# Kernel tuning notes

Measured on AMD Instinct MI355X. Metric: run time of the kernel, lower is better.

Reference implementation:

```python
import jax, jax.numpy as jnp
import numpy as np

EMBED_DIM = 1024
NUM_HEADS = 16
HEAD_DIM = EMBED_DIM // NUM_HEADS
KERNEL = 3
PAD = KERNEL // 2
B, L = 4, 1024


def conv1d(x, w, b):
    # x: [B, D, L], w: [D_out, D_in, K], b: [D_out]; 'same' padding like nn.Conv1d(padding=K//2)
    y = jax.lax.conv_general_dilated(
        x, w, window_strides=(1,), padding=[(PAD, PAD)],
        dimension_numbers=('NCH', 'OIH', 'NCH'))
    return y + b[None, :, None]


def setup_inputs() -> dict:
    key = jax.random.key(0)
    ks = jax.random.split(key, 12)
    fan = EMBED_DIM * KERNEL
    bound = 1.0 / np.sqrt(fan)
    def wconv(k):
        return jax.random.uniform(k, (EMBED_DIM, EMBED_DIM, KERNEL), jnp.float32, -bound, bound)
    def bconv(k):
        return jax.random.uniform(k, (EMBED_DIM,), jnp.float32, -bound, bound)
    return {
        'query': jax.random.normal(ks[0], (B, L, EMBED_DIM), jnp.float32),
        'key': jax.random.normal(ks[1], (B, L, EMBED_DIM), jnp.float32),
        'value': jax.random.normal(ks[2], (B, L, EMBED_DIM), jnp.float32),
        'key_padding_mask': jax.random.randint(ks[3], (B, L), 0, 2) > 0,
        'attn_mask': jnp.zeros((L, L), jnp.float32),
        'q_w': wconv(ks[4]), 'q_b': bconv(ks[5]),
        'k_w': wconv(ks[6]), 'k_b': bconv(ks[7]),
        'v_w': wconv(ks[8]), 'v_b': bconv(ks[9]),
        'o_w': wconv(ks[10]), 'o_b': bconv(ks[11]),
    }


def reference(query, key, value, key_padding_mask, attn_mask,
              q_w, q_b, k_w, k_b, v_w, v_b, o_w, o_b):
    scale = HEAD_DIM ** -0.5
    # projections: [B, D, L]
    q = conv1d(jnp.swapaxes(query, 1, 2), q_w, q_b)
    k = conv1d(jnp.swapaxes(key, 1, 2), k_w, k_b)
    v = conv1d(jnp.swapaxes(value, 1, 2), v_w, v_b)
    # [B, H, d, L]
    q = q.reshape(B, NUM_HEADS, HEAD_DIM, L)
    k = k.reshape(B, NUM_HEADS, HEAD_DIM, L)
    v = v.reshape(B, NUM_HEADS, HEAD_DIM, L)
    # scores: [B, H, L, L]
    scores = jnp.einsum('bhdi,bhdj->bhij', q, k) * scale
    scores = scores + attn_mask[None, None, :, :]
    scores = jnp.where(key_padding_mask[:, None, None, :], -jnp.inf, scores)
    attn = jax.nn.softmax(scores, axis=-1)  # dropout p=0 (eval) -> identity
    out = jnp.einsum('bhij,bhdj->bhdi', attn, v)  # [B, H, d, L]
    out = out.reshape(B, EMBED_DIM, L)
    out = conv1d(out, o_w, o_b)
    return jnp.swapaxes(out, 1, 2)  # [B, L, D]
```

## Files before the change

### kernel.cpp

```cpp
#include <hip/hip_runtime.h>
#include <math.h>

#define NB 4
#define NL 1024
#define ND 1024
#define NH 16
#define HD 64

typedef __attribute__((ext_vector_type(8))) short bf16x8;
typedef __attribute__((ext_vector_type(4))) float f32x4;

static __device__ __forceinline__ unsigned short f32_to_bf16(float f) {
  unsigned u = __float_as_uint(f);
  u += 0x7FFFu + ((u >> 16) & 1u);
  return (unsigned short)(u >> 16);
}
static __device__ __forceinline__ float bf16_to_f32(unsigned short s) {
  return __uint_as_float(((unsigned)s) << 16);
}

static __device__ __forceinline__ void split8(float4 a, float4 b, bf16x8* hi, bf16x8* lo) {
  unsigned u[8] = {__float_as_uint(a.x), __float_as_uint(a.y),
                   __float_as_uint(a.z), __float_as_uint(a.w),
                   __float_as_uint(b.x), __float_as_uint(b.y),
                   __float_as_uint(b.z), __float_as_uint(b.w)};
  union { unsigned p[4]; bf16x8 v; } H, L;
#pragma unroll
  for (int p = 0; p < 4; ++p) {
    unsigned u0 = u[2 * p], u1 = u[2 * p + 1];
    H.p[p] = __builtin_amdgcn_perm(u1, u0, 0x07060302u);
    unsigned l0 = __float_as_uint(__uint_as_float(u0) - __uint_as_float(u0 & 0xFFFF0000u));
    unsigned l1 = __float_as_uint(__uint_as_float(u1) - __uint_as_float(u1 & 0xFFFF0000u));
    L.p[p] = __builtin_amdgcn_perm(l1, l0, 0x07060302u);
  }
  *hi = H.v; *lo = L.v;
}

__global__ __launch_bounds__(256) void wcvt_kernel(
    const float* __restrict__ w0, const float* __restrict__ w1,
    const float* __restrict__ w2, const float* __restrict__ w3,
    unsigned short* __restrict__ wb, int* __restrict__ flag)
{
  if (blockIdx.x == 0 && blockIdx.y == 0 && threadIdx.x == 0) flag[0] = 0;
  const int t = blockIdx.y;
  const int o = blockIdx.x;
  const float* w = (t == 0) ? w0 : (t == 1) ? w1 : (t == 2) ? w2 : w3;
  unsigned short* hi = wb + (size_t)t * 6 * (1u << 20);
  unsigned short* lo = hi + 3 * (1u << 20);
  const int tid = threadIdx.x;
  float v[12];
  const float* src = w + (size_t)o * (ND * 3) + tid * 12;
#pragma unroll
  for (int j = 0; j < 3; ++j) {
    float4 f = *(const float4*)(src + j * 4);
    v[j * 4 + 0] = f.x; v[j * 4 + 1] = f.y; v[j * 4 + 2] = f.z; v[j * 4 + 3] = f.w;
  }
#pragma unroll
  for (int k = 0; k < 3; ++k) {
    unsigned short hh[4], ll[4];
#pragma unroll
    for (int ii = 0; ii < 4; ++ii) {
      float x = v[ii * 3 + k];
      unsigned short h = f32_to_bf16(x);
      float r = x - bf16_to_f32(h);
      hh[ii] = h; ll[ii] = f32_to_bf16(r);
    }
    size_t dst = (size_t)k * (ND * ND) + (size_t)o * ND + tid * 4;
    *(ushort4*)&hi[dst] = make_ushort4(hh[0], hh[1], hh[2], hh[3]);
    *(ushort4*)&lo[dst] = make_ushort4(ll[0], ll[1], ll[2], ll[3]);
  }
}

__global__ __launch_bounds__(256) void amask_scan(
    const float* __restrict__ a, int* __restrict__ flag)
{
  size_t i = ((size_t)blockIdx.x * 256 + threadIdx.x) * 4;
  float4 v = *(const float4*)&a[i];
  if (v.x != 0.f || v.y != 0.f || v.z != 0.f || v.w != 0.f) atomicOr(flag, 1);
}

__global__ __launch_bounds__(256, 3) void conv_mfma2(
    const float* X0, const float* X1, const float* X2,
    const unsigned short* __restrict__ wb,
    const float* b0, const float* b1, const float* b2,
    float* Y0, float* Y1, float* Y2, int mode)
{
  __shared__ float Af[128 * 32];
  __shared__ unsigned short Bh[128 * 32];
  __shared__ unsigned short Bl[128 * 32];

  const int tid = threadIdx.x, lane = tid & 63, wave = tid >> 6;
  const int lin = blockIdx.x + 8 * (blockIdx.y + 32 * blockIdx.z);
  const int g = lin & 7, t = lin >> 3;
  const int nb = (g & 3) * 2 + (t & 1);
  const int mb = (g >> 2) * 16 + ((t >> 1) & 15);
  const int z  = t >> 5;
  const int n0 = nb * 128, m0 = mb * 128;
  const int b = m0 >> 10, l0v = m0 & (NL - 1);

  const float* X = (mode == 0) ? (z == 0 ? X0 : (z == 1 ? X1 : X2)) : X0;
  const unsigned short* Wh = (mode == 0) ? wb + (size_t)z * 6 * (1u << 20) : wb;
  const unsigned short* Wl = Wh + 3 * (1u << 20);

  const int wm = (wave >> 1) * 64, wn = (wave & 1) * 64;
  const int mrow = lane & 15, quad = lane >> 4;
  const int r16 = lane >> 2, cs = lane & 3;
  const int src_chunk = (cs - (r16 >> 1)) & 3;
  const int bswz = ((quad + (mrow >> 1)) & 3) * 8;

  f32x4 acc[4][4] = {};

  const int kbeg = (mode == 0) ? 0 : z;
  const int kend = (mode == 0) ? 3 : z + 1;
  for (int koff = kbeg; koff < kend; ++koff) {
    const bool edge_lo = (l0v == 0 && koff == 0);
    const bool edge_hi = (l0v == NL - 128 && koff == 2);
    for (int i0 = 0; i0 < ND; i0 += 32) {
#pragma unroll
      for (int s = 0; s < 2; ++s) {
        const int seg = wave * 2 + s;
        const size_t goff = ((size_t)koff << 20) +
                            (size_t)(n0 + seg * 16 + r16) * ND + i0 + src_chunk * 8;
        __builtin_amdgcn_global_load_lds(
            (const __attribute__((address_space(1))) unsigned int*)(Wh + goff),
            (__attribute__((address_space(3))) unsigned int*)&Bh[seg * 512], 16, 0, 0);
        __builtin_amdgcn_global_load_lds(
            (const __attribute__((address_space(1))) unsigned int*)(Wl + goff),
            (__attribute__((address_space(3))) unsigned int*)&Bl[seg * 512], 16, 0, 0);
      }
#pragma unroll
      for (int j = 0; j < 4; ++j) {
        const int s = (wave * 4 + j) * 64 + lane;
        const int row = s >> 3, sir = s & 7;
        const int chunk = (sir - (row & 7)) & 7;
        int l = l0v + row + koff - 1;
        l = (l < 0) ? 0 : (l > NL - 1 ? NL - 1 : l);
        const float* gp = X + ((size_t)(b << 10) + l) * ND + i0 + chunk * 4;
        __builtin_amdgcn_global_load_lds(
            (const __attribute__((address_space(1))) unsigned int*)gp,
            (__attribute__((address_space(3))) unsigned int*)&Af[(wave * 4 + j) * 256],
            16, 0, 0);
      }
      __syncthreads();
      if (edge_lo || edge_hi) {
        const int er = edge_lo ? 0 : 127;
        if (tid < 8) *(float4*)&Af[er * 32 + tid * 4] = make_float4(0.f, 0.f, 0.f, 0.f);
        __syncthreads();
      }
      bf16x8 ah[4], al[4];
#pragma unroll
      for (int mi = 0; mi < 4; ++mi) {
        const int row = wm + mi * 16 + mrow, r7 = row & 7;
        float4 fa = *(const float4*)&Af[row * 32 + (((quad * 2) + r7) & 7) * 4];
        float4 fb = *(const float4*)&Af[row * 32 + (((quad * 2 + 1) + r7) & 7) * 4];
        split8(fa, fb, &ah[mi], &al[mi]);
      }
#pragma unroll
      for (int ni = 0; ni < 4; ++ni) {
        const int brow = wn + ni * 16 + mrow;
        bf16x8 bh = *(const bf16x8*)&Bh[brow * 32 + bswz];
        bf16x8 bl = *(const bf16x8*)&Bl[brow * 32 + bswz];
#pragma unroll
        for (int mi = 0; mi < 4; ++mi) {
          acc[mi][ni] = __builtin_amdgcn_mfma_f32_16x16x32_bf16(ah[mi], bh, acc[mi][ni], 0, 0, 0);
          acc[mi][ni] = __builtin_amdgcn_mfma_f32_16x16x32_bf16(ah[mi], bl, acc[mi][ni], 0, 0, 0);
          acc[mi][ni] = __builtin_amdgcn_mfma_f32_16x16x32_bf16(al[mi], bh, acc[mi][ni], 0, 0, 0);
        }
      }
      __syncthreads();
    }
  }

  if (mode == 0) {
    float* Y = (z == 0) ? Y0 : (z == 1 ? Y1 : Y2);
    const float* bias = (z == 0) ? b0 : (z == 1 ? b1 : b2);
#pragma unroll
    for (int ni = 0; ni < 4; ++ni) {
      const int n = n0 + wn + ni * 16 + mrow;
      const float bv = bias[n];
      const int h = n >> 6, dd = n & 63;
#pragma unroll
      for (int mi = 0; mi < 4; ++mi) {
        const int mbase = m0 + wm + mi * 16 + quad * 4;
        f32x4 v = acc[mi][ni];
#pragma unroll
        for (int r = 0; r < 4; ++r) {
          const int l = (mbase + r) & (NL - 1);
          Y[(((size_t)b * NH + h) * NL + l) * HD + dd] = v[r] + bv;
        }
      }
    }
  } else {
    float* P = Y0 + (size_t)z * ((size_t)NB * NL * ND);
#pragma unroll
    for (int ni = 0; ni < 4; ++ni) {
      const int n = n0 + wn + ni * 16 + mrow;
#pragma unroll
      for (int mi = 0; mi < 4; ++mi) {
        const int mbase = m0 + wm + mi * 16 + quad * 4;
        f32x4 v = acc[mi][ni];
#pragma unroll
        for (int r = 0; r < 4; ++r) {
          const int l = (mbase + r) & (NL - 1);
          P[((size_t)(b << 10) + l) * ND + n] = v[r];
        }
      }
    }
  }
}

__global__ __launch_bounds__(256) void reduce_kernel(
    const float* __restrict__ P, const float* __restrict__ bias, float* __restrict__ out)
{
  const size_t S = (size_t)NB * NL * ND;
  const size_t idx = ((size_t)blockIdx.x * 256 + threadIdx.x) * 4;
  const int n = (int)(idx & (ND - 1));
  float4 p0 = *(const float4*)&P[idx];
  float4 p1 = *(const float4*)&P[idx + S];
  float4 p2 = *(const float4*)&P[idx + 2 * S];
  float4 bv = *(const float4*)&bias[n];
  float4 r;
  r.x = p0.x + p1.x + p2.x + bv.x;
  r.y = p0.y + p1.y + p2.y + bv.y;
  r.z = p0.z + p1.z + p2.z + bv.z;
  r.w = p0.w + p1.w + p2.w + bv.w;
  *(float4*)&out[idx] = r;
}

__global__ __launch_bounds__(256, 3) void attn_mfma(
    const float* __restrict__ qT, const float* __restrict__ kT,
    const float* __restrict__ vT, const int* __restrict__ kpm,
    const float* __restrict__ amask, const int* __restrict__ aflagp,
    float* __restrict__ AO)
{
  __shared__ __align__(16) unsigned short S[3 * 64 * 72];
  unsigned short* Kh = S;
  unsigned short* Kl = S + 4608;
  unsigned short* Vt = S + 2 * 4608;

  const int tid = threadIdx.x, lane = tid & 63, wave = tid >> 6;
  const int c = lane & 15, quad = lane >> 4;
  const int lin = blockIdx.x;
  const int bh = (lin & 7) + 8 * (lin >> 7);
  const int mt = (lin >> 3) & 15;
  const int b = bh >> 4;
  const int m0 = mt * 64;
  const size_t base = (size_t)bh * NL * HD;
  const int aflag = *aflagp;
  const int mrow = wave * 16 + c;
  const int gm = m0 + mrow;

  const int sr = tid >> 2, scq = tid & 3;

#pragma unroll
  for (int ii = 0; ii < 2; ++ii) {
    const int c8 = scq * 2 + ii;
    const float* gp = &qT[base + (size_t)(m0 + sr) * HD + c8 * 8];
    float4 a = *(const float4*)gp, bb = *(const float4*)(gp + 4);
    a.x *= 0.125f; a.y *= 0.125f; a.z *= 0.125f; a.w *= 0.125f;
    bb.x *= 0.125f; bb.y *= 0.125f; bb.z *= 0.125f; bb.w *= 0.125f;
    bf16x8 hi, lo; split8(a, bb, &hi, &lo);
    const int cso = ((c8 + sr) & 7) * 8;
    *(bf16x8*)&Kh[sr * 72 + cso] = hi;
    *(bf16x8*)&Kl[sr * 72 + cso] = lo;
  }
  __syncthreads();
  bf16x8 qbh[2], qbl[2];
#pragma unroll
  for (int kb = 0; kb < 2; ++kb) {
    const int cso = ((kb * 4 + quad + mrow) & 7) * 8;
    qbh[kb] = *(const bf16x8*)&Kh[mrow * 72 + cso];
    qbl[kb] = *(const bf16x8*)&Kl[mrow * 72 + cso];
  }

  f32x4 acc[4] = {};
  float m_r = -INFINITY, l_r = 0.0f;

  for (int n0t = 0; n0t < NL; n0t += 64) {
    __syncthreads();

    float mval[4][4];
#pragma unroll
    for (int nf = 0; nf < 4; ++nf)
#pragma unroll
      for (int r = 0; r < 4; ++r) {
        const int gn = n0t + nf * 16 + quad * 4 + r;
        const bool pm = kpm[b * NL + gn] != 0;
        float am = 0.f;
        if (aflag) am = amask[(size_t)gm * NL + gn];
        mval[nf][r] = pm ? -INFINITY : am;
      }

#pragma unroll
    for (int ii = 0; ii < 2; ++ii) {
      const int c8 = scq * 2 + ii;
      const float* gp = &kT[base + (size_t)(n0t + sr) * HD + c8 * 8];
      float4 a = *(const float4*)gp, bb = *(const float4*)(gp + 4);
      bf16x8 hi, lo; split8(a, bb, &hi, &lo);
      const int cso = ((c8 + sr) & 7) * 8;
      *(bf16x8*)&Kh[sr * 72 + cso] = hi;
      *(bf16x8*)&Kl[sr * 72 + cso] = lo;

      const float* gv = &vT[base + (size_t)(n0t + sr) * HD + c8 * 8];
      float4 va = *(const float4*)gv, vb = *(const float4*)(gv + 4);
      float ve[8] = {va.x, va.y, va.z, va.w, vb.x, vb.y, vb.z, vb.w};
#pragma unroll
      for (int e = 0; e < 8; ++e) {
        const int dd = c8 * 8 + e;
        Vt[dd * 72 + (((sr >> 3) + dd) & 7) * 8 + (sr & 7)] = f32_to_bf16(ve[e]);
      }
    }
    __syncthreads();

    f32x4 sa[4] = {};
#pragma unroll
    for (int kb = 0; kb < 2; ++kb)
#pragma unroll
      for (int nf = 0; nf < 4; ++nf) {
        const int row = nf * 16 + c;
        const int cso = ((kb * 4 + quad + row) & 7) * 8;
        bf16x8 kah = *(const bf16x8*)&Kh[row * 72 + cso];
        bf16x8 kal = *(const bf16x8*)&Kl[row * 72 + cso];
        sa[nf] = __builtin_amdgcn_mfma_f32_16x16x32_bf16(kah, qbh[kb], sa[nf], 0, 0, 0);
        sa[nf] = __builtin_amdgcn_mfma_f32_16x16x32_bf16(kah, qbl[kb], sa[nf], 0, 0, 0);
        sa[nf] = __builtin_amdgcn_mfma_f32_16x16x32_bf16(kal, qbh[kb], sa[nf], 0, 0, 0);
      }

    float p[4][4];
    float tmax = -INFINITY;
#pragma unroll
    for (int nf = 0; nf < 4; ++nf)
#pragma unroll
      for (int r = 0; r < 4; ++r) {
        float s = sa[nf][r] + mval[nf][r];
        p[nf][r] = s;
        tmax = fmaxf(tmax, s);
      }
    tmax = fmaxf(tmax, __shfl_xor(tmax, 16));
    tmax = fmaxf(tmax, __shfl_xor(tmax, 32));
    const float newm = fmaxf(m_r, tmax);
    const float msafe = (newm == -INFINITY) ? 0.f : newm;
    const float alpha = __expf(m_r - msafe);
    float rs = 0.f;
#pragma unroll
    for (int nf = 0; nf < 4; ++nf)
#pragma unroll
      for (int r = 0; r < 4; ++r) {
        float e = __expf(p[nf][r] - msafe);
        p[nf][r] = e;
        rs += e;
      }
    rs += __shfl_xor(rs, 16);
    rs += __shfl_xor(rs, 32);
    l_r = l_r * alpha + rs;
    m_r = newm;
#pragma unroll
    for (int df = 0; df < 4; ++df) {
      acc[df][0] *= alpha; acc[df][1] *= alpha;
      acc[df][2] *= alpha; acc[df][3] *= alpha;
    }

    unsigned q16[4][2];
#pragma unroll
    for (int nf = 0; nf < 4; ++nf)
#pragma unroll
      for (int w = 0; w < 2; ++w)
        q16[nf][w] = (unsigned)f32_to_bf16(p[nf][2 * w]) |
                     ((unsigned)f32_to_bf16(p[nf][2 * w + 1]) << 16);

#pragma unroll
    for (int kb = 0; kb < 2; ++kb) {
      union { unsigned d[4]; bf16x8 v; } pb;
#pragma unroll
      for (int w = 0; w < 4; ++w) {
        const int addr = ((((quad & 1) * 2 + (w >> 1)) * 16 + c) << 2);
        unsigned v0 = __builtin_amdgcn_ds_bpermute(addr, (int)q16[2 * kb][w & 1]);
        unsigned v1 = __builtin_amdgcn_ds_bpermute(addr, (int)q16[2 * kb + 1][w & 1]);
        pb.d[w] = (quad >> 1) ? v1 : v0;
      }
#pragma unroll
      for (int df = 0; df < 4; ++df) {
        const int row = df * 16 + c;
        const int cso = ((kb * 4 + quad + row) & 7) * 8;
        bf16x8 va = *(const bf16x8*)&Vt[row * 72 + cso];
        acc[df] = __builtin_amdgcn_mfma_f32_16x16x32_bf16(va, pb.v, acc[df], 0, 0, 0);
      }
    }
  }

  __syncthreads();
  const float inv = 1.0f / l_r;
  float* Ob = (float*)S + wave * (16 * 68);
#pragma unroll
  for (int df = 0; df < 4; ++df)
#pragma unroll
    for (int r = 0; r < 4; ++r)
      Ob[c * 68 + df * 16 + quad * 4 + r] = acc[df][r] * inv;
  __syncthreads();
  const int mr2 = lane >> 2, cq2 = lane & 3;
  const int h = bh & 15;
#pragma unroll
  for (int ii = 0; ii < 4; ++ii) {
    const int chunk = cq2 * 4 + ii;
    float4 v = *(const float4*)&Ob[mr2 * 68 + chunk * 4];
    *(float4*)&AO[((size_t)(b << 10) + (m0 + wave * 16 + mr2)) * ND +
                  h * HD + chunk * 4] = v;
  }
}

extern "C" void kernel_launch(void* const* d_in, const int* in_sizes, int n_in,
                              void* d_out, int out_size, void* d_ws, size_t ws_size,
                              hipStream_t stream) {
  (void)in_sizes; (void)n_in; (void)out_size; (void)ws_size;
  const float* query = (const float*)d_in[0];
  const float* key_  = (const float*)d_in[1];
  const float* value = (const float*)d_in[2];
  const int*   kpm   = (const int*)d_in[3];
  const float* amask = (const float*)d_in[4];
  const float* q_w = (const float*)d_in[5];
  const float* q_b = (const float*)d_in[6];
  const float* k_w = (const float*)d_in[7];
  const float* k_b = (const float*)d_in[8];
  const float* v_w = (const float*)d_in[9];
  const float* v_b = (const float*)d_in[10];
  const float* o_w = (const float*)d_in[11];
  const float* o_b = (const float*)d_in[12];
  float* out = (float*)d_out;

  unsigned short* Wb = (unsigned short*)d_ws;
  float* qT = (float*)((char*)d_ws + (size_t)50331648);
  float* kT = qT + (size_t)NB * NL * ND;
  float* vT = kT + (size_t)NB * NL * ND;
  float* P  = qT;
  float* AO = (float*)d_ws;
  int* flag = (int*)d_out;

  wcvt_kernel<<<dim3(1024, 4), 256, 0, stream>>>(q_w, k_w, v_w, o_w, Wb, flag);
  amask_scan<<<1024, 256, 0, stream>>>(amask, flag);
  conv_mfma2<<<dim3(8, 32, 3), 256, 0, stream>>>(
      query, key_, value, Wb, q_b, k_b, v_b, qT, kT, vT, 0);
  attn_mfma<<<1024, 256, 0, stream>>>(qT, kT, vT, kpm, amask, flag, AO);
  conv_mfma2<<<dim3(8, 32, 3), 256, 0, stream>>>(
      AO, AO, AO, Wb + (size_t)3 * 6 * (1u << 20), o_b, o_b, o_b, P, P, P, 1);
  reduce_kernel<<<4096, 256, 0, stream>>>(P, o_b, out);
}
```

Baseline: 504.7 us.

## Pre-split activations into bf16 hi/lo buffers for conv and attention kernels

Adds a pre-pass that splits the input activations into padded bf16 hi/lo arrays, so the projection conv can load bf16 tiles straight into LDS instead of converting fp32 on every tile. The Q/K/V projection epilogue now writes split bf16 Q/K (with the softmax scale folded into Q) and bf16 V. Attention loads these directly with global_load_lds and writes its output as padded hi/lo bf16 for the output conv. The aim is to remove repeated fp32-to-bf16 splitting and halve activation traffic, at the cost of an extra split kernel, more workspace, and a branch on workspace size.

```diff
diff --git a/kernel.cpp b/kernel.cpp
--- a/kernel.cpp
+++ b/kernel.cpp
@@ -6,6 +6,7 @@
 #define ND 1024
 #define NH 16
 #define HD 64
+#define XS_ONE 4202496u
 
 typedef __attribute__((ext_vector_type(8))) short bf16x8;
 typedef __attribute__((ext_vector_type(4))) float f32x4;
@@ -18,7 +19,12 @@
 static __device__ __forceinline__ float bf16_to_f32(unsigned short s) {
   return __uint_as_float(((unsigned)s) << 16);
 }
-
+static __device__ __forceinline__ void split1(float x, unsigned short* h, unsigned short* l) {
+  unsigned u = __float_as_uint(x);
+  *h = (unsigned short)(u >> 16);
+  float r = x - __uint_as_float(u & 0xFFFF0000u);
+  *l = (unsigned short)(__float_as_uint(r) >> 16);
+}
 static __device__ __forceinline__ void split8(float4 a, float4 b, bf16x8* hi, bf16x8* lo) {
   unsigned u[8] = {__float_as_uint(a.x), __float_as_uint(a.y),
                    __float_as_uint(a.z), __float_as_uint(a.w),
@@ -79,15 +85,43 @@
   if (v.x != 0.f || v.y != 0.f || v.z != 0.f || v.w != 0.f) atomicOr(flag, 1);
 }
 
-__global__ __launch_bounds__(256, 3) void conv_mfma2(
+__global__ __launch_bounds__(256) void xsplit_kernel(
+    const float* __restrict__ x0, const float* __restrict__ x1,
+    const float* __restrict__ x2, unsigned short* __restrict__ XS)
+{
+  const int r = blockIdx.x;
+  const int b = blockIdx.y;
+  const int t = blockIdx.z;
+  unsigned short* hi = XS + (size_t)t * 2 * XS_ONE;
+  unsigned short* lo = hi + XS_ONE;
+  const size_t o = ((size_t)b * 1026 + r) * ND + threadIdx.x * 4;
+  if (r == 0 || r == 1025) {
+    ushort4 z = make_ushort4(0, 0, 0, 0);
+    *(ushort4*)&hi[o] = z; *(ushort4*)&lo[o] = z;
+    return;
+  }
+  const float* x = (t == 0) ? x0 : (t == 1) ? x1 : x2;
+  float4 f = *(const float4*)&x[((size_t)b * NL + (r - 1)) * ND + threadIdx.x * 4];
+  unsigned short hs[4], ls[4];
+  split1(f.x, &hs[0], &ls[0]); split1(f.y, &hs[1], &ls[1]);
+  split1(f.z, &hs[2], &ls[2]); split1(f.w, &hs[3], &ls[3]);
+  *(ushort4*)&hi[o] = make_ushort4(hs[0], hs[1], hs[2], hs[3]);
+  *(ushort4*)&lo[o] = make_ushort4(ls[0], ls[1], ls[2], ls[3]);
+}
+
+template <int MODE, bool PRE>
+__global__ __launch_bounds__(256, 3) void conv_mfma3(
     const float* X0, const float* X1, const float* X2,
+    const unsigned short* __restrict__ XS,
     const unsigned short* __restrict__ wb,
     const float* b0, const float* b1, const float* b2,
-    float* Y0, float* Y1, float* Y2, int mode)
+    unsigned short* qh, unsigned short* ql,
+    unsigned short* kh, unsigned short* kl, unsigned short* vv,
+    float* P)
 {
-  __shared__ float Af[128 * 32];
-  __shared__ unsigned short Bh[128 * 32];
-  __shared__ unsigned short Bl[128 * 32];
+  __shared__ __align__(16) unsigned short AS[8192];
+  __shared__ __align__(16) unsigned short Bh[4096];
+  __shared__ __align__(16) unsigned short Bl[4096];
 
   const int tid = threadIdx.x, lane = tid & 63, wave = tid >> 6;
   const int lin = blockIdx.x + 8 * (blockIdx.y + 32 * blockIdx.z);
@@ -98,9 +132,14 @@
   const int n0 = nb * 128, m0 = mb * 128;
   const int b = m0 >> 10, l0v = m0 & (NL - 1);
 
-  const float* X = (mode == 0) ? (z == 0 ? X0 : (z == 1 ? X1 : X2)) : X0;
-  const unsigned short* Wh = (mode == 0) ? wb + (size_t)z * 6 * (1u << 20) : wb;
+  const unsigned short* Wh = (MODE == 0) ? wb + (size_t)z * 6 * (1u << 20) : wb;
   const unsigned short* Wl = Wh + 3 * (1u << 20);
+  const unsigned short* Xh = nullptr;
+  const unsigned short* Xl = nullptr;
+  const float* X = nullptr;
+  if (MODE == 1) { Xh = XS; Xl = XS + XS_ONE; }
+  else if (PRE)  { Xh = XS + (size_t)z * 2 * XS_ONE; Xl = Xh + XS_ONE; }
+  else           { X = (z == 0) ? X0 : (z == 1) ? X1 : X2; }
 
   const int wm = (wave >> 1) * 64, wn = (wave & 1) * 64;
   const int mrow = lane & 15, quad = lane >> 4;
@@ -110,11 +149,12 @@
 
   f32x4 acc[4][4] = {};
 
-  const int kbeg = (mode == 0) ? 0 : z;
-  const int kend = (mode == 0) ? 3 : z + 1;
+  const int kbeg = (MODE == 0) ? 0 : z;
+  const int kend = (MODE == 0) ? 3 : z + 1;
   for (int koff = kbeg; koff < kend; ++koff) {
-    const bool edge_lo = (l0v == 0 && koff == 0);
-    const bool edge_hi = (l0v == NL - 128 && koff == 2);
+    const bool edge_lo = (!PRE) && (l0v == 0 && koff == 0);
+    const bool edge_hi = (!PRE) && (l0v == NL - 128 && koff == 2);
+    const int rowbase = b * 1026 + l0v + koff;
     for (int i0 = 0; i0 < ND; i0 += 32) {
 #pragma unroll
       for (int s = 0; s < 2; ++s) {
@@ -128,32 +168,59 @@
             (const __attribute__((address_space(1))) unsigned int*)(Wl + goff),
             (__attribute__((address_space(3))) unsigned int*)&Bl[seg * 512], 16, 0, 0);
       }
-#pragma unroll
-      for (int j = 0; j < 4; ++j) {
-        const int s = (wave * 4 + j) * 64 + lane;
-        const int row = s >> 3, sir = s & 7;
-        const int chunk = (sir - (row & 7)) & 7;
-        int l = l0v + row + koff - 1;
-        l = (l < 0) ? 0 : (l > NL - 1 ? NL - 1 : l);
-        const float* gp = X + ((size_t)(b << 10) + l) * ND + i0 + chunk * 4;
-        __builtin_amdgcn_global_load_lds(
-            (const __attribute__((address_space(1))) unsigned int*)gp,
-            (__attribute__((address_space(3))) unsigned int*)&Af[(wave * 4 + j) * 256],
-            16, 0, 0);
-      }
-      __syncthreads();
-      if (edge_lo || edge_hi) {
-        const int er = edge_lo ? 0 : 127;
-        if (tid < 8) *(float4*)&Af[er * 32 + tid * 4] = make_float4(0.f, 0.f, 0.f, 0.f);
+      if (MODE == 1 || PRE) {
+#pragma unroll
+        for (int s = 0; s < 2; ++s) {
+          const int seg = wave * 2 + s;
+          const size_t goff = (size_t)(rowbase + seg * 16 + r16) * ND + i0 + src_chunk * 8;
+          __builtin_amdgcn_global_load_lds(
+              (const __attribute__((address_space(1))) unsigned int*)(Xh + goff),
+              (__attribute__((address_space(3))) unsigned int*)&AS[seg * 512], 16, 0, 0);
+          __builtin_amdgcn_global_load_lds(
+              (const __attribute__((address_space(1))) unsigned int*)(Xl + goff),
+              (__attribute__((address_space(3))) unsigned int*)&AS[4096 + seg * 512], 16, 0, 0);
+        }
         __syncthreads();
-      }
+      } else {
+        float* Af = (float*)AS;
+#pragma unroll
+        for (int j = 0; j < 4; ++j) {
+          const int s = (wave * 4 + j) * 64 + lane;
+          const int row = s >> 3, sir = s & 7;
+          const int chunk = (sir - (row & 7)) & 7;
+          int l = l0v + row + koff - 1;
+          l = (l < 0) ? 0 : (l > NL - 1 ? NL - 1 : l);
+          const float* gp = X + ((size_t)(b << 10) + l) * ND + i0 + chunk * 4;
+          __builtin_amdgcn_global_load_lds(
+              (const __attribute__((address_space(1))) unsigned int*)gp,
+              (__attribute__((address_space(3))) unsigned int*)&Af[(wave * 4 + j) * 256],
+              16, 0, 0);
+        }
+        __syncthreads();
+        if (edge_lo || edge_hi) {
+          const int er = edge_lo ? 0 : 127;
+          if (tid < 8) *(float4*)&Af[er * 32 + tid * 4] = make_float4(0.f, 0.f, 0.f, 0.f);
+          __syncthreads();
+        }
+      }
+
       bf16x8 ah[4], al[4];
-#pragma unroll
-      for (int mi = 0; mi < 4; ++mi) {
-        const int row = wm + mi * 16 + mrow, r7 = row & 7;
-        float4 fa = *(const float4*)&Af[row * 32 + (((quad * 2) + r7) & 7) * 4];
-        float4 fb = *(const float4*)&Af[row * 32 + (((quad * 2 + 1) + r7) & 7) * 4];
-        split8(fa, fb, &ah[mi], &al[mi]);
+      if (MODE == 1 || PRE) {
+#pragma unroll
+        for (int mi = 0; mi < 4; ++mi) {
+          const int row = wm + mi * 16 + mrow;
+          ah[mi] = *(const bf16x8*)&AS[row * 32 + bswz];
+          al[mi] = *(const bf16x8*)&AS[4096 + row * 32 + bswz];
+        }
+      } else {
+        const float* Af = (const float*)AS;
+#pragma unroll
+        for (int mi = 0; mi < 4; ++mi) {
+          const int row = wm + mi * 16 + mrow, r7 = row & 7;
+          float4 fa = *(const float4*)&Af[row * 32 + (((quad * 2) + r7) & 7) * 4];
+          float4 fb = *(const float4*)&Af[row * 32 + (((quad * 2 + 1) + r7) & 7) * 4];
+          split8(fa, fb, &ah[mi], &al[mi]);
+        }
       }
 #pragma unroll
       for (int ni = 0; ni < 4; ++ni) {
@@ -171,14 +238,13 @@
     }
   }
 
-  if (mode == 0) {
-    float* Y = (z == 0) ? Y0 : (z == 1 ? Y1 : Y2);
-    const float* bias = (z == 0) ? b0 : (z == 1 ? b1 : b2);
+  if (MODE == 0) {
+    const float* bias = (z == 0) ? b0 : (z == 1) ? b1 : b2;
 #pragma unroll
     for (int ni = 0; ni < 4; ++ni) {
       const int n = n0 + wn + ni * 16 + mrow;
       const float bv = bias[n];
-      const int h = n >> 6, dd = n & 63;
+      const int h2 = n >> 6, dd = n & 63;
 #pragma unroll
       for (int mi = 0; mi < 4; ++mi) {
         const int mbase = m0 + wm + mi * 16 + quad * 4;
@@ -186,12 +252,23 @@
 #pragma unroll
         for (int r = 0; r < 4; ++r) {
           const int l = (mbase + r) & (NL - 1);
-          Y[(((size_t)b * NH + h) * NL + l) * HD + dd] = v[r] + bv;
+          const size_t o = (((size_t)b * NH + h2) * NL + l) * HD + dd;
+          float val = v[r] + bv;
+          if (z == 0) {
+            val *= 0.125f;
+            unsigned short hs, ls; split1(val, &hs, &ls);
+            qh[o] = hs; ql[o] = ls;
+          } else if (z == 1) {
+            unsigned short hs, ls; split1(val, &hs, &ls);
+            kh[o] = hs; kl[o] = ls;
+          } else {
+            vv[o] = f32_to_bf16(val);
+          }
         }
       }
     }
   } else {
-    float* P = Y0 + (size_t)z * ((size_t)NB * NL * ND);
+    float* Pz = P + (size_t)z * ((size_t)NB * NL * ND);
 #pragma unroll
     for (int ni = 0; ni < 4; ++ni) {
       const int n = n0 + wn + ni * 16 + mrow;
@@ -202,7 +279,7 @@
 #pragma unroll
         for (int r = 0; r < 4; ++r) {
           const int l = (mbase + r) & (NL - 1);
-          P[((size_t)(b << 10) + l) * ND + n] = v[r];
+          Pz[((size_t)(b << 10) + l) * ND + n] = v[r];
         }
       }
     }
@@ -227,87 +304,104 @@
   *(float4*)&out[idx] = r;
 }
 
-__global__ __launch_bounds__(256, 3) void attn_mfma(
-    const float* __restrict__ qT, const float* __restrict__ kT,
-    const float* __restrict__ vT, const int* __restrict__ kpm,
+__global__ __launch_bounds__(256, 3) void attn_mfma2(
+    const unsigned short* __restrict__ qhp, const unsigned short* __restrict__ qlp,
+    const unsigned short* __restrict__ khp, const unsigned short* __restrict__ klp,
+    const unsigned short* __restrict__ vvp, const int* __restrict__ kpm,
     const float* __restrict__ amask, const int* __restrict__ aflagp,
-    float* __restrict__ AO)
+    unsigned short* __restrict__ AOh, unsigned short* __restrict__ AOl)
 {
-  __shared__ __align__(16) unsigned short S[3 * 64 * 72];
-  unsigned short* Kh = S;
-  unsigned short* Kl = S + 4608;
-  unsigned short* Vt = S + 2 * 4608;
+  __shared__ __align__(16) unsigned short SM[8192 + 4608];
+  unsigned short* Kh = SM;
+  unsigned short* Kl = SM + 4096;
+  unsigned short* Vt = SM + 8192;
 
   const int tid = threadIdx.x, lane = tid & 63, wave = tid >> 6;
   const int c = lane & 15, quad = lane >> 4;
   const int lin = blockIdx.x;
   const int bh = (lin & 7) + 8 * (lin >> 7);
   const int mt = (lin >> 3) & 15;
-  const int b = bh >> 4;
+  const int b = bh >> 4, h = bh & 15;
   const int m0 = mt * 64;
-  const size_t base = (size_t)bh * NL * HD;
+  const size_t base = (size_t)bh * (NL * HD);
   const int aflag = *aflagp;
   const int mrow = wave * 16 + c;
   const int gm = m0 + mrow;
 
-  const int sr = tid >> 2, scq = tid & 3;
-
-#pragma unroll
-  for (int ii = 0; ii < 2; ++ii) {
-    const int c8 = scq * 2 + ii;
-    const float* gp = &qT[base + (size_t)(m0 + sr) * HD + c8 * 8];
-    float4 a = *(const float4*)gp, bb = *(const float4*)(gp + 4);
-    a.x *= 0.125f; a.y *= 0.125f; a.z *= 0.125f; a.w *= 0.125f;
-    bb.x *= 0.125f; bb.y *= 0.125f; bb.z *= 0.125f; bb.w *= 0.125f;
-    bf16x8 hi, lo; split8(a, bb, &hi, &lo);
-    const int cso = ((c8 + sr) & 7) * 8;
-    *(bf16x8*)&Kh[sr * 72 + cso] = hi;
-    *(bf16x8*)&Kl[sr * 72 + cso] = lo;
+  if (h == 0 && mt == 0) {
+    ushort4 z4 = make_ushort4(0, 0, 0, 0);
+    *(ushort4*)&AOh[(size_t)(b * 1026) * ND + tid * 4] = z4;
+    *(ushort4*)&AOl[(size_t)(b * 1026) * ND + tid * 4] = z4;
+  }
+  if (h == 0 && mt == 15) {
+    ushort4 z4 = make_ushort4(0, 0, 0, 0);
+    *(ushort4*)&AOh[((size_t)(b * 1026) + 1025) * ND + tid * 4] = z4;
+    *(ushort4*)&AOl[((size_t)(b * 1026) + 1025) * ND + tid * 4] = z4;
+  }
+
+  const int rowo = lane >> 3;
+  const int grano = ((lane & 7) - rowo) & 7;
+
+#pragma unroll
+  for (int j = 0; j < 2; ++j) {
+    const int s = wave * 2 + j;
+    const size_t go = base + (size_t)(m0 + s * 8 + rowo) * HD + grano * 8;
+    __builtin_amdgcn_global_load_lds(
+        (const __attribute__((address_space(1))) unsigned int*)(qhp + go),
+        (__attribute__((address_space(3))) unsigned int*)&Kh[s * 512], 16, 0, 0);
+    __builtin_amdgcn_global_load_lds(
+        (const __attribute__((address_space(1))) unsigned int*)(qlp + go),
+        (__attribute__((address_space(3))) unsigned int*)&Kl[s * 512], 16, 0, 0);
   }
   __syncthreads();
   bf16x8 qbh[2], qbl[2];
 #pragma unroll
   for (int kb = 0; kb < 2; ++kb) {
     const int cso = ((kb * 4 + quad + mrow) & 7) * 8;
-    qbh[kb] = *(const bf16x8*)&Kh[mrow * 72 + cso];
-    qbl[kb] = *(const bf16x8*)&Kl[mrow * 72 + cso];
+    qbh[kb] = *(const bf16x8*)&Kh[mrow * 64 + cso];
+    qbl[kb] = *(const bf16x8*)&Kl[mrow * 64 + cso];
   }
 
   f32x4 acc[4] = {};
   float m_r = -INFINITY, l_r = 0.0f;
+  const int sr = tid >> 2, scq = tid & 3;
 
   for (int n0t = 0; n0t < NL; n0t += 64) {
     __syncthreads();
 
     float mval[4][4];
 #pragma unroll
-    for (int nf = 0; nf < 4; ++nf)
+    for (int nf = 0; nf < 4; ++nf) {
+      int4 pm4 = *(const int4*)&kpm[b * NL + n0t + nf * 16 + quad * 4];
+      const int* pmi = &pm4.x;
 #pragma unroll
       for (int r = 0; r < 4; ++r) {
-        const int gn = n0t + nf * 16 + quad * 4 + r;
-        const bool pm = kpm[b * NL + gn] != 0;
         float am = 0.f;
-        if (aflag) am = amask[(size_t)gm * NL + gn];
-        mval[nf][r] = pm ? -INFINITY : am;
-      }
-
+        if (aflag) am = amask[(size_t)gm * NL + (n0t + nf * 16 + quad * 4 + r)];
+        mval[nf][r] = pmi[r] ? -INFINITY : am;
+      }
+    }
+
+#pragma unroll
+    for (int j = 0; j < 2; ++j) {
+      const int s = wave * 2 + j;
+      const size_t go = base + (size_t)(n0t + s * 8 + rowo) * HD + grano * 8;
+      __builtin_amdgcn_global_load_lds(
+          (const __attribute__((address_space(1))) unsigned int*)(khp + go),
+          (__attribute__((address_space(3))) unsigned int*)&Kh[s * 512], 16, 0, 0);
+      __builtin_amdgcn_global_load_lds(
+          (const __attribute__((address_space(1))) unsigned int*)(klp + go),
+          (__attribute__((address_space(3))) unsigned int*)&Kl[s * 512], 16, 0, 0);
+    }
 #pragma unroll
     for (int ii = 0; ii < 2; ++ii) {
       const int c8 = scq * 2 + ii;
-      const float* gp = &kT[base + (size_t)(n0t + sr) * HD + c8 * 8];
-      float4 a = *(const float4*)gp, bb = *(const float4*)(gp + 4);
-      bf16x8 hi, lo; split8(a, bb, &hi, &lo);
-      const int cso = ((c8 + sr) & 7) * 8;
-      *(bf16x8*)&Kh[sr * 72 + cso] = hi;
-      *(bf16x8*)&Kl[sr * 72 + cso] = lo;
-
-      const float* gv = &vT[base + (size_t)(n0t + sr) * HD + c8 * 8];
-      float4 va = *(const float4*)gv, vb = *(const float4*)(gv + 4);
-      float ve[8] = {va.x, va.y, va.z, va.w, vb.x, vb.y, vb.z, vb.w};
+      uint4 u = *(const uint4*)(vvp + base + (size_t)(n0t + sr) * HD + c8 * 8);
+      const unsigned short* pe = (const unsigned short*)&u;
 #pragma unroll
       for (int e = 0; e < 8; ++e) {
         const int dd = c8 * 8 + e;
-        Vt[dd * 72 + (((sr >> 3) + dd) & 7) * 8 + (sr & 7)] = f32_to_bf16(ve[e]);
+        Vt[dd * 72 + (((sr >> 3) + dd) & 7) * 8 + (sr & 7)] = pe[e];
       }
     }
     __syncthreads();
@@ -319,8 +413,8 @@
       for (int nf = 0; nf < 4; ++nf) {
         const int row = nf * 16 + c;
         const int cso = ((kb * 4 + quad + row) & 7) * 8;
-        bf16x8 kah = *(const bf16x8*)&Kh[row * 72 + cso];
-        bf16x8 kal = *(const bf16x8*)&Kl[row * 72 + cso];
+        bf16x8 kah = *(const bf16x8*)&Kh[row * 64 + cso];
+        bf16x8 kal = *(const bf16x8*)&Kl[row * 64 + cso];
         sa[nf] = __builtin_amdgcn_mfma_f32_16x16x32_bf16(kah, qbh[kb], sa[nf], 0, 0, 0);
         sa[nf] = __builtin_amdgcn_mfma_f32_16x16x32_bf16(kah, qbl[kb], sa[nf], 0, 0, 0);
         sa[nf] = __builtin_amdgcn_mfma_f32_16x16x32_bf16(kal, qbh[kb], sa[nf], 0, 0, 0);
@@ -367,7 +461,6 @@
       for (int w = 0; w < 2; ++w)
         q16[nf][w] = (unsigned)f32_to_bf16(p[nf][2 * w]) |
                      ((unsigned)f32_to_bf16(p[nf][2 * w + 1]) << 16);
-
 #pragma unroll
     for (int kb = 0; kb < 2; ++kb) {
       union { unsigned d[4]; bf16x8 v; } pb;
@@ -390,7 +483,7 @@
 
   __syncthreads();
   const float inv = 1.0f / l_r;
-  float* Ob = (float*)S + wave * (16 * 68);
+  float* Ob = (float*)SM + wave * (16 * 68);
 #pragma unroll
   for (int df = 0; df < 4; ++df)
 #pragma unroll
@@ -398,20 +491,24 @@
       Ob[c * 68 + df * 16 + quad * 4 + r] = acc[df][r] * inv;
   __syncthreads();
   const int mr2 = lane >> 2, cq2 = lane & 3;
-  const int h = bh & 15;
 #pragma unroll
   for (int ii = 0; ii < 4; ++ii) {
     const int chunk = cq2 * 4 + ii;
     float4 v = *(const float4*)&Ob[mr2 * 68 + chunk * 4];
-    *(float4*)&AO[((size_t)(b << 10) + (m0 + wave * 16 + mr2)) * ND +
-                  h * HD + chunk * 4] = v;
+    unsigned short hs[4], ls[4];
+    split1(v.x, &hs[0], &ls[0]); split1(v.y, &hs[1], &ls[1]);
+    split1(v.z, &hs[2], &ls[2]); split1(v.w, &hs[3], &ls[3]);
+    const size_t o = ((size_t)(b * 1026) + (m0 + wave * 16 + mr2) + 1) * ND +
+                     h * HD + chunk * 4;
+    *(ushort4*)&AOh[o] = make_ushort4(hs[0], hs[1], hs[2], hs[3]);
+    *(ushort4*)&AOl[o] = make_ushort4(ls[0], ls[1], ls[2], ls[3]);
   }
 }
 
 extern "C" void kernel_launch(void* const* d_in, const int* in_sizes, int n_in,
                               void* d_out, int out_size, void* d_ws, size_t ws_size,
                               hipStream_t stream) {
-  (void)in_sizes; (void)n_in; (void)out_size; (void)ws_size;
+  (void)in_sizes; (void)n_in; (void)out_size;
   const float* query = (const float*)d_in[0];
   const float* key_  = (const float*)d_in[1];
   const float* value = (const float*)d_in[2];
@@ -427,20 +524,34 @@
   const float* o_b = (const float*)d_in[12];
   float* out = (float*)d_out;
 
+  const size_t WB_BYTES = 50331648;
   unsigned short* Wb = (unsigned short*)d_ws;
-  float* qT = (float*)((char*)d_ws + (size_t)50331648);
-  float* kT = qT + (size_t)NB * NL * ND;
-  float* vT = kT + (size_t)NB * NL * ND;
-  float* P  = qT;
-  float* AO = (float*)d_ws;
+  const bool big = ws_size >= 142704640ull;
+  unsigned short* XSp = (unsigned short*)((char*)d_ws + WB_BYTES);
+  char* qkv_base = big ? ((char*)d_ws + 100761600) : ((char*)d_ws + WB_BYTES);
+  unsigned short* qh = (unsigned short*)qkv_base;
+  unsigned short* ql = qh + 4194304;
+  unsigned short* kh = ql + 4194304;
+  unsigned short* kl = kh + 4194304;
+  unsigned short* vv = kl + 4194304;
+  unsigned short* AOh = (unsigned short*)d_ws;
+  unsigned short* AOl = AOh + XS_ONE;
+  float* P = (float*)((char*)d_ws + WB_BYTES);
   int* flag = (int*)d_out;
 
   wcvt_kernel<<<dim3(1024, 4), 256, 0, stream>>>(q_w, k_w, v_w, o_w, Wb, flag);
   amask_scan<<<1024, 256, 0, stream>>>(amask, flag);
-  conv_mfma2<<<dim3(8, 32, 3), 256, 0, stream>>>(
-      query, key_, value, Wb, q_b, k_b, v_b, qT, kT, vT, 0);
-  attn_mfma<<<1024, 256, 0, stream>>>(qT, kT, vT, kpm, amask, flag, AO);
-  conv_mfma2<<<dim3(8, 32, 3), 256, 0, stream>>>(
-      AO, AO, AO, Wb + (size_t)3 * 6 * (1u << 20), o_b, o_b, o_b, P, P, P, 1);
+  if (big) {
+    xsplit_kernel<<<dim3(1026, NB, 3), 256, 0, stream>>>(query, key_, value, XSp);
+    conv_mfma3<0, true><<<dim3(8, 32, 3), 256, 0, stream>>>(
+        nullptr, nullptr, nullptr, XSp, Wb, q_b, k_b, v_b, qh, ql, kh, kl, vv, nullptr);
+  } else {
+    conv_mfma3<0, false><<<dim3(8, 32, 3), 256, 0, stream>>>(
+        query, key_, value, nullptr, Wb, q_b, k_b, v_b, qh, ql, kh, kl, vv, nullptr);
+  }
+  attn_mfma2<<<1024, 256, 0, stream>>>(qh, ql, kh, kl, vv, kpm, amask, flag, AOh, AOl);
+  conv_mfma3<1, true><<<dim3(8, 32, 3), 256, 0, stream>>>(
+      nullptr, nullptr, nullptr, AOh, Wb + (size_t)3 * 6 * (1u << 20),
+      nullptr, nullptr, nullptr, nullptr, nullptr, nullptr, nullptr, nullptr, P);
   reduce_kernel<<<4096, 256, 0, stream>>>(P, o_b, out);
 }
```

After: 521.6 us. 1.03x slower.
